# Kernel optimization log

Hardware: AMD Instinct MI355X
Metric: run time of the kernel (lower is better)

The kernel has to match this reference:

```python
import jax, jax.numpy as jnp
import numpy as np

CHUNK = 64
EPS = 1e-5


def segsum(a):
    # a: (..., T) -> (..., T, T) lower-triangular cumulative segment sums; -inf above diag
    T = a.shape[-1]
    cs = jnp.cumsum(a, axis=-1)
    ss = cs[..., :, None] - cs[..., None, :]
    mask = jnp.tril(jnp.ones((T, T), dtype=bool))
    return jnp.where(mask, ss, -jnp.inf)


def ssd(x, A, B, C, chunk):
    # x: (b, L, h, p), A: (b, L, h), B/C: (b, L, n)
    b, L, h, p = x.shape
    c = L // chunk
    x = x.reshape(b, c, chunk, h, p)
    A = A.reshape(b, c, chunk, h).transpose(0, 3, 1, 2)          # b h c l
    B = B.reshape(b, c, chunk, -1)                               # b c l n
    C = C.reshape(b, c, chunk, -1)                               # b c l n
    A_cum = jnp.cumsum(A, axis=-1)                               # b h c l
    Lmat = jnp.exp(segsum(A))                                    # b h c l l (causal decay)
    # intra-chunk (diagonal-block) output
    Y_diag = jnp.einsum('bcln,bcsn,bhcls,bcshp->bclhp', C, B, Lmat, x)
    # per-chunk states
    decay_states = jnp.exp(A_cum[..., -1:] - A_cum)              # b h c l
    states = jnp.einsum('bcln,bhcl,bclhp->bchpn', B, decay_states, x)
    states = jnp.concatenate([jnp.zeros_like(states[:, :1]), states], axis=1)  # b (c+1) h p n
    # inter-chunk recurrence via chunk-level segsum
    A_last = jnp.pad(A_cum[..., -1], ((0, 0), (0, 0), (1, 0)))   # b h (c+1)
    decay_chunk = jnp.exp(segsum(A_last))                        # b h (c+1) (c+1)
    new_states = jnp.einsum('bhzc,bchpn->bzhpn', decay_chunk, states)
    states, final = new_states[:, :-1], new_states[:, -1:]
    Y_off = jnp.einsum('bcln,bchpn,bhcl->bclhp', C, states, jnp.exp(A_cum))
    return (Y_diag + Y_off).reshape(b, L, h, p), final


def mamba2(x, W_in, conv_w, conv_b, dt_bias, A_log, D, norm_w, W_out):
    d_inner = norm_w.shape[0]
    nheads = dt_bias.shape[0]
    d_state = (conv_b.shape[0] - d_inner) // 2
    headdim = d_inner // nheads
    k_conv = conv_w.shape[0]
    b, L, _ = x.shape

    zxbcdt = x @ W_in                                            # (b, L, 2*d_inner+2*n+h)
    z = zxbcdt[..., :d_inner]
    xBC = zxbcdt[..., d_inner:2 * d_inner + 2 * d_state]
    dt = jax.nn.softplus(zxbcdt[..., 2 * d_inner + 2 * d_state:] + dt_bias)  # (b, L, h)
    A = -jnp.exp(A_log)                                          # (h,)

    # causal depthwise conv (zero init conv state == left-pad k_conv-1 zeros) + silu
    xp = jnp.pad(xBC, ((0, 0), (k_conv - 1, 0), (0, 0)))
    xBC = jax.lax.conv_general_dilated(
        xp, conv_w, (1,), 'VALID',
        dimension_numbers=('NWC', 'WIO', 'NWC'),
        feature_group_count=conv_b.shape[0])
    xBC = jax.nn.silu(xBC + conv_b)

    xs = xBC[..., :d_inner].reshape(b, L, nheads, headdim)       # (b, L, h, p)
    Bm = xBC[..., d_inner:d_inner + d_state]                     # (b, L, n)
    Cm = xBC[..., d_inner + d_state:]                            # (b, L, n)

    Y, _ = ssd(xs * dt[..., None], A * dt, Bm, Cm, CHUNK)
    Y = Y + xs * D                                               # D: (h, 1) broadcasts over p
    y = Y.reshape(b, L, d_inner)

    # gated RMSNorm
    y = y * jax.nn.silu(z)
    y = y * jax.lax.rsqrt(jnp.mean(y * y, axis=-1, keepdims=True) + EPS) * norm_w
    return y @ W_out


def setup_inputs():
    key = jax.random.key(0)
    ks = jax.random.split(key, 8)
    B, L, d_model = 2, 4096, 1024
    expand, d_state, k_conv, headdim = 2, 128, 4, 64
    d_inner = expand * d_model
    nheads = d_inner // headdim
    d_in_proj = 2 * d_inner + 2 * d_state + nheads
    conv_dim = d_inner + 2 * d_state
    return {
        'x': jax.random.normal(ks[0], (B, L, d_model), jnp.float32),
        'W_in': jax.random.normal(ks[1], (d_model, d_in_proj), jnp.float32) / np.sqrt(d_model).astype(np.float32),
        'conv_w': jax.random.normal(ks[2], (k_conv, 1, conv_dim), jnp.float32) / np.sqrt(k_conv).astype(np.float32),
        'conv_b': jnp.zeros((conv_dim,), jnp.float32),
        'dt_bias': jax.random.normal(ks[3], (nheads,), jnp.float32) * 0.5 - 2.0,
        'A_log': jnp.log(1.0 + 15.0 * jax.random.uniform(ks[4], (nheads,), jnp.float32)),
        'D': jax.random.normal(ks[5], (nheads, 1), jnp.float32),
        'norm_w': jnp.ones((d_inner,), jnp.float32),
        'W_out': jax.random.normal(ks[6], (d_inner, d_model), jnp.float32) / np.sqrt(d_inner).astype(np.float32),
    }


def reference(x, W_in, conv_w, conv_b, dt_bias, A_log, D, norm_w, W_out):
    return mamba2(x, W_in, conv_w, conv_b, dt_bias, A_log, D, norm_w, W_out)
```

## Files before the change

### kernel.cpp

```cpp
#include <hip/hip_runtime.h>
#include <hip/hip_fp16.h>

typedef _Float16 f16;
typedef _Float16 f16x4 __attribute__((ext_vector_type(4)));
typedef _Float16 f16x8 __attribute__((ext_vector_type(8)));
typedef float f32x4 __attribute__((ext_vector_type(4)));

#define DEV __device__ __forceinline__

constexpr int BB    = 2;
constexpr int LL    = 4096;
constexpr int DM    = 1024;
constexpr int DIN   = 2048;
constexpr int DST   = 128;
constexpr int NH    = 32;
constexpr int HD    = 64;
constexpr int NC    = 64;
constexpr int MROWS = BB * LL;
constexpr int NPROJ = 2*DIN + 2*DST + NH;
constexpr int NZ    = 2*DIN + 2*DST;
constexpr int CONVD = DIN + 2*DST;
constexpr int DT_OFF = 2*DIN + 2*DST;
constexpr int BOFF  = DIN;
constexpr int COFF  = DIN + DST;

DEV float silu_f(float v) { return v / (1.f + __expf(-v)); }

DEV void gload_lds16(const f16* gsrc, f16* lds_dst) {
  __builtin_amdgcn_global_load_lds(
      (const __attribute__((address_space(1))) void*)gsrc,
      (__attribute__((address_space(3))) void*)lds_dst, 16, 0, 0);
}

__global__ __launch_bounds__(256)
void tof16_kernel(const float* __restrict__ src, f16* __restrict__ dst, int n8) {
  int i = blockIdx.x * 256 + threadIdx.x;
  if (i >= n8) return;
  f32x4 a = *(const f32x4*)(src + (size_t)i*8);
  f32x4 b = *(const f32x4*)(src + (size_t)i*8 + 4);
  f16x8 o;
#pragma unroll
  for (int j = 0; j < 4; ++j) { o[j] = (f16)a[j]; o[4+j] = (f16)b[j]; }
  *(f16x8*)(dst + (size_t)i*8) = o;
}

__global__ __launch_bounds__(256)
void transpose_f32_to_f16(const float* __restrict__ src, f16* __restrict__ dst,
                          int K, int N, int srcLd) {
  __shared__ float tbuf[32][33];
  int n0 = blockIdx.x * 32, k0 = blockIdx.y * 32;
  int tx = threadIdx.x & 31, ty = threadIdx.x >> 5;
  for (int i = ty; i < 32; i += 8)
    tbuf[i][tx] = src[(size_t)(k0 + i)*srcLd + n0 + tx];
  __syncthreads();
  for (int i = ty; i < 32; i += 8)
    dst[(size_t)(n0 + i)*K + (k0 + tx)] = (f16)tbuf[tx][i];
}

template<int BM, int BN, int WM_, int WN_, bool C16>
__global__ __launch_bounds__(WM_*WN_*64, 2)
void gemm_t(const f16* __restrict__ A, const f16* __restrict__ Bt,
            void* __restrict__ Cp, int M, int N, int K, int ldc) {
  constexpr int THREADS = WM_*WN_*64;
  constexpr int WTM = BM/WM_, WTN = BN/WN_;
  constexpr int FM = WTM/16, FN = WTN/16;
  constexpr int LA = BM*4/THREADS, LB = BN*4/THREADS;
  constexpr int L = LA + LB;
  __shared__ f16 As[3][BM*32];
  __shared__ f16 Bs[3][BN*32];
  const int nbn = N / BN;
  const int bm = blockIdx.x / nbn, bn = blockIdx.x % nbn;
  const int tid = threadIdx.x;
  const int wave = tid >> 6, lane = tid & 63;
  const int lrow = lane & 15, kgrp = lane >> 4;
  const int wm = wave / WN_, wn = wave % WN_;
  const int nt = K >> 5;
  const int bcol8 = (kgrp ^ ((lrow ^ (lrow >> 2)) & 3)) * 8;

  const f16* aptr[LA];
  const f16* bptr[LB];
#pragma unroll
  for (int i = 0; i < LA; ++i) {
    int s = tid + i*THREADS, row = s >> 2;
    int g = (s & 3) ^ ((row ^ (row >> 2)) & 3);
    aptr[i] = A + (size_t)(bm*BM + row)*K + g*8;
  }
#pragma unroll
  for (int i = 0; i < LB; ++i) {
    int s = tid + i*THREADS, row = s >> 2;
    int g = (s & 3) ^ ((row ^ (row >> 2)) & 3);
    bptr[i] = Bt + (size_t)(bn*BN + row)*K + g*8;
  }

  f32x4 acc[FM][FN] = {};

  auto STAGE = [&](int buf, int t) {
#pragma unroll
    for (int i = 0; i < LA; ++i)
      gload_lds16(aptr[i] + (size_t)t*32, As[buf] + (wave*64 + i*THREADS)*8);
#pragma unroll
    for (int i = 0; i < LB; ++i)
      gload_lds16(bptr[i] + (size_t)t*32, Bs[buf] + (wave*64 + i*THREADS)*8);
  };
  auto WAITL = [&]() {
    if constexpr (L == 2)      asm volatile("s_waitcnt vmcnt(2)" ::: "memory");
    else if constexpr (L == 3) asm volatile("s_waitcnt vmcnt(3)" ::: "memory");
    else if constexpr (L == 4) asm volatile("s_waitcnt vmcnt(4)" ::: "memory");
    else if constexpr (L == 6) asm volatile("s_waitcnt vmcnt(6)" ::: "memory");
    else                       asm volatile("s_waitcnt vmcnt(0)" ::: "memory");
  };

  STAGE(0, 0);
  if (nt > 1) { STAGE(1, 1); WAITL(); }
  else        { asm volatile("s_waitcnt vmcnt(0)" ::: "memory"); }
  __builtin_amdgcn_s_barrier();
  __builtin_amdgcn_sched_barrier(0);

  for (int t = 0; t < nt; ++t) {
    const int cur = t % 3;
    if (t + 2 < nt) STAGE((t + 2) % 3, t + 2);
    const f16* Ab = As[cur];
    const f16* Bb = Bs[cur];
    f16x8 bf[FN];
#pragma unroll
    for (int n = 0; n < FN; ++n)
      bf[n] = *(const f16x8*)(Bb + (wn*WTN + n*16 + lrow)*32 + bcol8);
#pragma unroll
    for (int m = 0; m < FM; ++m) {
      f16x8 af = *(const f16x8*)(Ab + (wm*WTM + m*16 + lrow)*32 + bcol8);
#pragma unroll
      for (int n = 0; n < FN; ++n)
        acc[m][n] = __builtin_amdgcn_mfma_f32_16x16x32_f16(af, bf[n], acc[m][n], 0, 0, 0);
    }
    if (t + 1 < nt) {
      if (t + 2 < nt) WAITL();
      else            asm volatile("s_waitcnt vmcnt(0)" ::: "memory");
      __builtin_amdgcn_s_barrier();
      __builtin_amdgcn_sched_barrier(0);
    }
  }

  int crow0 = bm*BM + wm*WTM, ccol0 = bn*BN + wn*WTN;
#pragma unroll
  for (int m = 0; m < FM; ++m)
#pragma unroll
    for (int n = 0; n < FN; ++n) {
      int r0 = crow0 + m*16 + (lane >> 4)*4;
      int c0 = ccol0 + n*16 + (lane & 15);
#pragma unroll
      for (int r = 0; r < 4; ++r) {
        if constexpr (C16) {
          f16* C = (f16*)Cp;
          C[(size_t)(r0 + r)*ldc + c0] = (f16)acc[m][n][r];
        } else {
          float* C = (float*)Cp;
          C[(size_t)(r0 + r)*ldc + c0] = acc[m][n][r];
        }
      }
    }
}

__global__ __launch_bounds__(256)
void dt_kernel(const float* __restrict__ x, const float* __restrict__ Win,
               const float* __restrict__ dt_bias, const float* __restrict__ A_log,
               float* __restrict__ dt, float* __restrict__ Acum) {
  __shared__ float xs[64][132];
  __shared__ float ws[128][32];
  __shared__ float dts[64][32];
  int bc = blockIdx.x;
  int r0 = bc * 64;
  int t = threadIdx.x;
  int r = t >> 2, c0 = (t & 3) * 8;
  float acc[8] = {};
  for (int kt = 0; kt < 1024; kt += 128) {
    __syncthreads();
#pragma unroll
    for (int i = 0; i < 8; ++i) {
      int idx4 = t + i*256;
      int rr = idx4 >> 5, c4 = (idx4 & 31) * 4;
      *(f32x4*)&xs[rr][c4] = *(const f32x4*)(x + (size_t)(r0 + rr)*1024 + kt + c4);
    }
#pragma unroll
    for (int i = 0; i < 4; ++i) {
      int idx4 = t + i*256;
      int rr = idx4 >> 3, c4 = (idx4 & 7) * 4;
      *(f32x4*)&ws[rr][c4] = *(const f32x4*)(Win + (size_t)(kt + rr)*NPROJ + DT_OFF + c4);
    }
    __syncthreads();
#pragma unroll 8
    for (int k = 0; k < 128; ++k) {
      float xv = xs[r][k];
      f32x4 w0 = *(const f32x4*)&ws[k][c0];
      f32x4 w1 = *(const f32x4*)&ws[k][c0 + 4];
#pragma unroll
      for (int j = 0; j < 4; ++j) { acc[j] += xv * w0[j]; acc[4+j] += xv * w1[j]; }
    }
  }
#pragma unroll
  for (int j = 0; j < 8; ++j) {
    float v = acc[j] + dt_bias[c0 + j];
    float sp = (v > 20.f) ? v : log1pf(__expf(v));
    dt[(size_t)(r0 + r)*NH + c0 + j] = sp;
    dts[r][c0 + j] = sp;
  }
  __syncthreads();
  int wave = t >> 6, lane = t & 63;
  for (int hh = 0; hh < 8; ++hh) {
    int h = wave*8 + hh;
    float A = -__expf(A_log[h]);
    float v = A * dts[lane][h];
#pragma unroll
    for (int off = 1; off < 64; off <<= 1) {
      float u = __shfl_up(v, off);
      if (lane >= off) v += u;
    }
    Acum[((size_t)bc*NH + h)*64 + lane] = v;
  }
}

__global__ __launch_bounds__(256)
void conv_kernel(const f16* __restrict__ zxh, const float* __restrict__ cw,
                 const float* __restrict__ cb, f16* __restrict__ out) {
  int i = blockIdx.x * 256 + threadIdx.x;
  int row = i / (CONVD/8);
  int c8  = (i - row*(CONVD/8)) * 8;
  int lb = row & (LL - 1);
  f32x4 a0 = *(const f32x4*)(cb + c8);
  f32x4 a1 = *(const f32x4*)(cb + c8 + 4);
#pragma unroll
  for (int j = 0; j < 4; ++j) {
    int lsrc = lb - 3 + j;
    if (lsrc >= 0) {
      f16x8 v = *(const f16x8*)(zxh + (size_t)(row - 3 + j)*NZ + BOFF + c8);
      f32x4 w0 = *(const f32x4*)(cw + j*CONVD + c8);
      f32x4 w1 = *(const f32x4*)(cw + j*CONVD + c8 + 4);
#pragma unroll
      for (int jj = 0; jj < 4; ++jj) {
        a0[jj] += (float)v[jj]   * w0[jj];
        a1[jj] += (float)v[4+jj] * w1[jj];
      }
    }
  }
  f16x8 o;
#pragma unroll
  for (int jj = 0; jj < 4; ++jj) {
    o[jj]   = (f16)silu_f(a0[jj]);
    o[4+jj] = (f16)silu_f(a1[jj]);
  }
  *(f16x8*)(out + (size_t)row*CONVD + c8) = o;
}

__global__ __launch_bounds__(256)
void gbuf_kernel(const f16* __restrict__ xbc, f16* __restrict__ G) {
  __shared__ float Cs[64][128];
  __shared__ float Bsm[64][128];
  int bc = blockIdx.x;
  int row0 = bc * 64;
  int t = threadIdx.x;
#pragma unroll
  for (int i = 0; i < 4; ++i) {
    int idx = t + i*256;
    int r = idx >> 4, c8 = (idx & 15) * 8;
    f16x8 cv = *(const f16x8*)(xbc + (size_t)(row0 + r)*CONVD + COFF + c8);
    f16x8 bv = *(const f16x8*)(xbc + (size_t)(row0 + r)*CONVD + BOFF + c8);
    f32x4 c0v = {(float)cv[0], (float)cv[1], (float)cv[2], (float)cv[3]};
    f32x4 c1v = {(float)cv[4], (float)cv[5], (float)cv[6], (float)cv[7]};
    f32x4 b0v = {(float)bv[0], (float)bv[1], (float)bv[2], (float)bv[3]};
    f32x4 b1v = {(float)bv[4], (float)bv[5], (float)bv[6], (float)bv[7]};
    *(f32x4*)&Cs[r][c8]      = c0v;  *(f32x4*)&Cs[r][c8 + 4]  = c1v;
    *(f32x4*)&Bsm[r][c8]     = b0v;  *(f32x4*)&Bsm[r][c8 + 4] = b1v;
  }
  __syncthreads();
  int l0 = (t >> 4)*4, s0 = (t & 15)*4;
  float acc[4][4] = {};
  for (int n4 = 0; n4 < 128; n4 += 4) {
    f32x4 cv[4], bv[4];
#pragma unroll
    for (int i = 0; i < 4; ++i) cv[i] = *(const f32x4*)&Cs[l0 + i][n4];
#pragma unroll
    for (int j = 0; j < 4; ++j) bv[j] = *(const f32x4*)&Bsm[s0 + j][n4];
#pragma unroll
    for (int i = 0; i < 4; ++i)
#pragma unroll
      for (int j = 0; j < 4; ++j)
        acc[i][j] += cv[i][0]*bv[j][0] + cv[i][1]*bv[j][1] + cv[i][2]*bv[j][2] + cv[i][3]*bv[j][3];
  }
#pragma unroll
  for (int i = 0; i < 4; ++i) {
    f16x4 v = {(f16)acc[i][0], (f16)acc[i][1], (f16)acc[i][2], (f16)acc[i][3]};
    *(f16x4*)(G + ((size_t)bc*64 + l0 + i)*64 + s0) = v;
  }
}

__global__ __launch_bounds__(256)
void ssd_states_kernel(const f16* __restrict__ xbc, const float* __restrict__ dtb,
                       const float* __restrict__ Acum, f16* __restrict__ states) {
  __shared__ union {
    struct { f16 XdT[64][72]; f16 BT[128][72]; } s;
    float Sl[64][132];
  } u;
  __shared__ float ac[64], dts[64];
  int bc = blockIdx.x >> 5, h = blockIdx.x & 31;
  int row0 = bc*64, t = threadIdx.x;
  if (t < 64) {
    ac[t]  = Acum[((size_t)bc*NH + h)*64 + t];
    dts[t] = dtb[(size_t)(row0 + t)*NH + h];
  }
  __syncthreads();
  float ac63 = ac[63];
#pragma unroll
  for (int i = 0; i < 2; ++i) {
    int idx = t + i*256; int l = idx >> 3, p8 = (idx & 7)*8;
    f16x8 v = *(const f16x8*)(xbc + (size_t)(row0 + l)*CONVD + h*HD + p8);
    float d = dts[l];
#pragma unroll
    for (int j = 0; j < 8; ++j) u.s.XdT[p8 + j][l] = (f16)((float)v[j]*d);
  }
#pragma unroll
  for (int i = 0; i < 4; ++i) {
    int idx = t + i*256; int l = idx >> 4, n8 = (idx & 15)*8;
    f16x8 v = *(const f16x8*)(xbc + (size_t)(row0 + l)*CONVD + BOFF + n8);
    float dl = __expf(ac63 - ac[l]);
#pragma unroll
    for (int j = 0; j < 8; ++j) u.s.BT[n8 + j][l] = (f16)((float)v[j]*dl);
  }
  __syncthreads();
  int wave = t >> 6, lane = t & 63;
  int lrow = lane & 15, kgrp = lane >> 4;
  f32x4 sacc[8] = {};
#pragma unroll
  for (int kk = 0; kk < 64; kk += 32) {
    f16x8 afs = *(const f16x8*)&u.s.XdT[wave*16 + lrow][kk + kgrp*8];
#pragma unroll
    for (int n = 0; n < 8; ++n) {
      f16x8 bf = *(const f16x8*)&u.s.BT[n*16 + lrow][kk + kgrp*8];
      sacc[n] = __builtin_amdgcn_mfma_f32_16x16x32_f16(afs, bf, sacc[n], 0, 0, 0);
    }
  }
  __syncthreads();
#pragma unroll
  for (int n = 0; n < 8; ++n)
#pragma unroll
    for (int r = 0; r < 4; ++r)
      u.Sl[wave*16 + kgrp*4 + r][n*16 + lrow] = sacc[n][r];
  __syncthreads();
  size_t sb = ((size_t)bc*NH + h)*8192;
#pragma unroll
  for (int i = 0; i < 4; ++i) {
    int idx = t + i*256; int p = idx >> 4, n8 = (idx & 15)*8;
    f16x8 o;
#pragma unroll
    for (int j = 0; j < 8; ++j) o[j] = (f16)u.Sl[p][n8 + j];
    *(f16x8*)(states + sb + (size_t)p*128 + n8) = o;
  }
}

__global__ __launch_bounds__(256)
void scan_kernel(f16* __restrict__ states, const float* __restrict__ Acum) {
  int bid = blockIdx.x;
  int bh = bid >> 3, pgrp = bid & 7;
  int b = bh >> 5, h = bh & 31;
  int t = threadIdx.x;
  int p = pgrp*8 + (t >> 5), n4 = (t & 31) * 4;
  size_t off = (size_t)p*128 + n4;
  f32x4 carry = {0.f, 0.f, 0.f, 0.f};
  for (int c = 0; c < NC; ++c) {
    size_t base = ((size_t)(b*NC + c)*NH + h)*8192;
    f16x4 cv = *(f16x4*)(states + base + off);
    f16x4 st;
#pragma unroll
    for (int j = 0; j < 4; ++j) st[j] = (f16)carry[j];
    *(f16x4*)(states + base + off) = st;
    float tc = __expf(Acum[((size_t)(b*NC + c)*NH + h)*64 + 63]);
#pragma unroll
    for (int j = 0; j < 4; ++j) carry[j] = carry[j]*tc + (float)cv[j];
  }
}

__global__ __launch_bounds__(256)
void yoff_kernel(const f16* __restrict__ xbc, const f16* __restrict__ zxh,
                 const f16* __restrict__ Gg, const f16* __restrict__ states,
                 const float* __restrict__ dtb, const float* __restrict__ Acum,
                 const float* __restrict__ Dp, f16* __restrict__ Ybuf) {
  __shared__ union {
    struct { f16 Gt[64][72]; f16 XdT[64][72]; } a;
    struct { f16 Ch[64][136]; f16 Sin[64][136]; } b;
    float Yl2[64][68];
  } u;
  __shared__ float Yl[64][68];
  __shared__ float ac[64], dts[64], eac[64];
  int bc = blockIdx.x >> 5, h = blockIdx.x & 31;
  int row0 = bc*64, t = threadIdx.x;
  if (t < 64) {
    float a0 = Acum[((size_t)bc*NH + h)*64 + t];
    ac[t]  = a0;
    eac[t] = __expf(a0);
    dts[t] = dtb[(size_t)(row0 + t)*NH + h];
  }
  __syncthreads();
#pragma unroll
  for (int i = 0; i < 2; ++i) {
    int idx = t + i*256; int l = idx >> 3, p8 = (idx & 7)*8;
    f16x8 v = *(const f16x8*)(xbc + (size_t)(row0 + l)*CONVD + h*HD + p8);
    float d = dts[l];
#pragma unroll
    for (int j = 0; j < 8; ++j) u.a.XdT[p8 + j][l] = (f16)((float)v[j]*d);
  }
#pragma unroll
  for (int i = 0; i < 2; ++i) {
    int idx = t + i*256; int l = idx >> 3, s8 = (idx & 7)*8;
    f16x8 g = *(const f16x8*)(Gg + (size_t)bc*4096 + l*64 + s8);
    float al = ac[l];
    f16x8 o;
#pragma unroll
    for (int j = 0; j < 8; ++j) {
      int s = s8 + j;
      o[j] = (l >= s) ? (f16)((float)g[j] * __expf(al - ac[s])) : (f16)0.f;
    }
    *(f16x8*)&u.a.Gt[l][s8] = o;
  }
  __syncthreads();
  int wave = t >> 6, lane = t & 63;
  int lrow = lane & 15, kgrp = lane >> 4;
  f32x4 yacc[4] = {};
#pragma unroll
  for (int kk = 0; kk < 64; kk += 32) {
    f16x8 afy = *(const f16x8*)&u.a.Gt[wave*16 + lrow][kk + kgrp*8];
#pragma unroll
    for (int n = 0; n < 4; ++n) {
      f16x8 bf = *(const f16x8*)&u.a.XdT[n*16 + lrow][kk + kgrp*8];
      yacc[n] = __builtin_amdgcn_mfma_f32_16x16x32_f16(afy, bf, yacc[n], 0, 0, 0);
    }
  }
  __syncthreads();
#pragma unroll
  for (int n = 0; n < 4; ++n)
#pragma unroll
    for (int r = 0; r < 4; ++r)
      Yl[wave*16 + kgrp*4 + r][n*16 + lrow] = yacc[n][r];
  size_t sb = ((size_t)bc*NH + h)*8192;
#pragma unroll
  for (int i = 0; i < 4; ++i) {
    int idx = t + i*256; int r = idx >> 4, c8 = (idx & 15)*8;
    *(f16x8*)&u.b.Ch[r][c8]  = *(const f16x8*)(xbc + (size_t)(row0 + r)*CONVD + COFF + c8);
    *(f16x8*)&u.b.Sin[r][c8] = *(const f16x8*)(states + sb + (size_t)r*128 + c8);
  }
  __syncthreads();
  f32x4 acc[4] = {};
#pragma unroll
  for (int kk = 0; kk < 128; kk += 32) {
    f16x8 af = *(const f16x8*)&u.b.Ch[wave*16 + lrow][kk + kgrp*8];
#pragma unroll
    for (int n = 0; n < 4; ++n) {
      f16x8 bf = *(const f16x8*)&u.b.Sin[n*16 + lrow][kk + kgrp*8];
      acc[n] = __builtin_amdgcn_mfma_f32_16x16x32_f16(af, bf, acc[n], 0, 0, 0);
    }
  }
  __syncthreads();
#pragma unroll
  for (int n = 0; n < 4; ++n)
#pragma unroll
    for (int r = 0; r < 4; ++r)
      u.Yl2[wave*16 + kgrp*4 + r][n*16 + lrow] = acc[n][r];
  __syncthreads();
  float Dh = Dp[h];
#pragma unroll
  for (int i = 0; i < 2; ++i) {
    int idx = t + i*256; int l = idx >> 3, p8 = (idx & 7)*8;
    int row = row0 + l;
    f16x8 zh = *(const f16x8*)(zxh + (size_t)row*NZ + h*HD + p8);
    f16x8 xs = *(const f16x8*)(xbc + (size_t)row*CONVD + h*HD + p8);
    float e = eac[l];
    f16x8 o;
#pragma unroll
    for (int j = 0; j < 8; ++j) {
      float yv = Yl[l][p8 + j] + e*u.Yl2[l][p8 + j] + (float)xs[j]*Dh;
      o[j] = (f16)(yv * silu_f((float)zh[j]));
    }
    *(f16x8*)(Ybuf + (size_t)row*DIN + h*HD + p8) = o;
  }
}

__global__ __launch_bounds__(256)
void rms_kernel(const f16* __restrict__ yg, const float* __restrict__ nw,
                f16* __restrict__ yh) {
  __shared__ float red[4];
  int row = blockIdx.x, t = threadIdx.x;
  f16x8 v = *(const f16x8*)(yg + (size_t)row*DIN + t*8);
  float f[8];
  float ss = 0.f;
#pragma unroll
  for (int j = 0; j < 8; ++j) { f[j] = (float)v[j]; ss += f[j]*f[j]; }
#pragma unroll
  for (int off = 32; off > 0; off >>= 1) ss += __shfl_down(ss, off);
  if ((t & 63) == 0) red[t >> 6] = ss;
  __syncthreads();
  float tot = red[0] + red[1] + red[2] + red[3];
  float sc = rsqrtf(tot * (1.f/2048.f) + 1e-5f);
  f32x4 w0 = *(const f32x4*)(nw + t*8);
  f32x4 w1 = *(const f32x4*)(nw + t*8 + 4);
  f16x8 o;
#pragma unroll
  for (int j = 0; j < 4; ++j) {
    o[j]   = (f16)(f[j]   * sc * w0[j]);
    o[4+j] = (f16)(f[4+j] * sc * w1[j]);
  }
  *(f16x8*)(yh + (size_t)row*DIN + t*8) = o;
}

extern "C" void kernel_launch(void* const* d_in, const int* in_sizes, int n_in,
                              void* d_out, int out_size, void* d_ws, size_t ws_size,
                              hipStream_t stream) {
  const float* x       = (const float*)d_in[0];
  const float* W_in    = (const float*)d_in[1];
  const float* conv_w  = (const float*)d_in[2];
  const float* conv_b  = (const float*)d_in[3];
  const float* dt_bias = (const float*)d_in[4];
  const float* A_log   = (const float*)d_in[5];
  const float* Dp      = (const float*)d_in[6];
  const float* norm_w  = (const float*)d_in[7];
  const float* W_out   = (const float*)d_in[8];

  constexpr size_t WS_NEED = 213909504;
  if (ws_size < WS_NEED) return;

  char* w = (char*)d_ws;
  f16*   states = (f16*)(w + 0);
  f16*   winT   = (f16*)(w + 0);
  f16*   yh     = (f16*)(w + 0);
  f16*   xh     = (f16*)(w + 33554432);
  f16*   woutT  = (f16*)(w + 33554432);
  f16*   zxh    = (f16*)(w + 67108864);
  f16*   xbcc   = (f16*)(w + 138412032);
  f16*   Ybuf   = (f16*)(w + 176160768);
  float* dtb    = (float*)(w + 209715200);
  float* Acum   = (float*)(w + 210763776);
  f16*   Gg     = (f16*)(w + 211812352);

  tof16_kernel<<<4096, 256, 0, stream>>>(x, xh, MROWS*DM/8);
  transpose_f32_to_f16<<<dim3(NZ/32, DM/32), 256, 0, stream>>>(W_in, winT, DM, NZ, NPROJ);
  gemm_t<256,128,4,2,true><<<(MROWS/256)*(NZ/128), 512, 0, stream>>>(xh, winT, zxh, MROWS, NZ, DM, NZ);
  dt_kernel<<<MROWS/64, 256, 0, stream>>>(x, W_in, dt_bias, A_log, dtb, Acum);
  conv_kernel<<<MROWS*(CONVD/8)/256, 256, 0, stream>>>(zxh, conv_w, conv_b, xbcc);
  gbuf_kernel<<<BB*NC, 256, 0, stream>>>(xbcc, Gg);
  ssd_states_kernel<<<BB*NC*NH, 256, 0, stream>>>(xbcc, dtb, Acum, states);
  scan_kernel<<<BB*NH*8, 256, 0, stream>>>(states, Acum);
  yoff_kernel<<<BB*NC*NH, 256, 0, stream>>>(xbcc, zxh, Gg, states, dtb, Acum, Dp, Ybuf);
  transpose_f32_to_f16<<<dim3(DM/32, DIN/32), 256, 0, stream>>>(W_out, woutT, DIN, DM, DM);
  rms_kernel<<<MROWS, 256, 0, stream>>>(Ybuf, norm_w, yh);
  gemm_t<128,128,2,2,false><<<(MROWS/128)*(DM/128), 256, 0, stream>>>(yh, woutT, d_out, MROWS, DM, DIN, DM);
}
```

Baseline: 434.9 us.

## Fold RMSNorm weight into W_out and row scale into GEMM epilogue; remap GEMM blocks

The norm weight is folded into the transposed W_out, and the RMS normalization becomes a per-row scale applied in the output GEMM's epilogue. The rms kernel now only computes the scale, so the normalized f16 copy of Y is no longer written and re-read. Both GEMMs also remap block indices with an interleave across groups of 8 workgroups, probably to spread neighbouring tiles across XCDs or improve cache locality. The GEMM now reads the unnormalized f16 Y, which is a small numeric difference, and the epilogue does an extra scale load per row.

```diff
diff --git a/kernel.cpp b/kernel.cpp
--- a/kernel.cpp
+++ b/kernel.cpp
@@ -46,21 +46,23 @@
 
 __global__ __launch_bounds__(256)
 void transpose_f32_to_f16(const float* __restrict__ src, f16* __restrict__ dst,
-                          int K, int N, int srcLd) {
+                          int K, int N, int srcLd, const float* __restrict__ colScale) {
   __shared__ float tbuf[32][33];
   int n0 = blockIdx.x * 32, k0 = blockIdx.y * 32;
   int tx = threadIdx.x & 31, ty = threadIdx.x >> 5;
   for (int i = ty; i < 32; i += 8)
     tbuf[i][tx] = src[(size_t)(k0 + i)*srcLd + n0 + tx];
   __syncthreads();
+  float cs = colScale ? colScale[k0 + tx] : 1.f;
   for (int i = ty; i < 32; i += 8)
-    dst[(size_t)(n0 + i)*K + (k0 + tx)] = (f16)tbuf[tx][i];
+    dst[(size_t)(n0 + i)*K + (k0 + tx)] = (f16)(tbuf[tx][i] * cs);
 }
 
 template<int BM, int BN, int WM_, int WN_, bool C16>
 __global__ __launch_bounds__(WM_*WN_*64, 2)
 void gemm_t(const f16* __restrict__ A, const f16* __restrict__ Bt,
-            void* __restrict__ Cp, int M, int N, int K, int ldc) {
+            void* __restrict__ Cp, int M, int N, int K, int ldc,
+            const float* __restrict__ rowScale) {
   constexpr int THREADS = WM_*WN_*64;
   constexpr int WTM = BM/WM_, WTN = BN/WN_;
   constexpr int FM = WTM/16, FN = WTN/16;
@@ -69,7 +71,9 @@
   __shared__ f16 As[3][BM*32];
   __shared__ f16 Bs[3][BN*32];
   const int nbn = N / BN;
-  const int bm = blockIdx.x / nbn, bn = blockIdx.x % nbn;
+  const int nwg = (int)gridDim.x;
+  const int lb  = ((int)blockIdx.x & 7) * (nwg >> 3) + ((int)blockIdx.x >> 3);
+  const int bm = lb / nbn, bn = lb % nbn;
   const int tid = threadIdx.x;
   const int wave = tid >> 6, lane = tid & 63;
   const int lrow = lane & 15, kgrp = lane >> 4;
@@ -149,12 +153,14 @@
       int c0 = ccol0 + n*16 + (lane & 15);
 #pragma unroll
       for (int r = 0; r < 4; ++r) {
+        float v = acc[m][n][r];
+        if (rowScale) v *= rowScale[r0 + r];
         if constexpr (C16) {
           f16* C = (f16*)Cp;
-          C[(size_t)(r0 + r)*ldc + c0] = (f16)acc[m][n][r];
+          C[(size_t)(r0 + r)*ldc + c0] = (f16)v;
         } else {
           float* C = (float*)Cp;
-          C[(size_t)(r0 + r)*ldc + c0] = acc[m][n][r];
+          C[(size_t)(r0 + r)*ldc + c0] = v;
         }
       }
     }
@@ -482,30 +488,21 @@
 }
 
 __global__ __launch_bounds__(256)
-void rms_kernel(const f16* __restrict__ yg, const float* __restrict__ nw,
-                f16* __restrict__ yh) {
+void rms_scale_kernel(const f16* __restrict__ yg, float* __restrict__ scale) {
   __shared__ float red[4];
   int row = blockIdx.x, t = threadIdx.x;
   f16x8 v = *(const f16x8*)(yg + (size_t)row*DIN + t*8);
-  float f[8];
   float ss = 0.f;
 #pragma unroll
-  for (int j = 0; j < 8; ++j) { f[j] = (float)v[j]; ss += f[j]*f[j]; }
+  for (int j = 0; j < 8; ++j) { float f = (float)v[j]; ss += f*f; }
 #pragma unroll
   for (int off = 32; off > 0; off >>= 1) ss += __shfl_down(ss, off);
   if ((t & 63) == 0) red[t >> 6] = ss;
   __syncthreads();
-  float tot = red[0] + red[1] + red[2] + red[3];
-  float sc = rsqrtf(tot * (1.f/2048.f) + 1e-5f);
-  f32x4 w0 = *(const f32x4*)(nw + t*8);
-  f32x4 w1 = *(const f32x4*)(nw + t*8 + 4);
-  f16x8 o;
-#pragma unroll
-  for (int j = 0; j < 4; ++j) {
-    o[j]   = (f16)(f[j]   * sc * w0[j]);
-    o[4+j] = (f16)(f[4+j] * sc * w1[j]);
-  }
-  *(f16x8*)(yh + (size_t)row*DIN + t*8) = o;
+  if (t == 0) {
+    float tot = red[0] + red[1] + red[2] + red[3];
+    scale[row] = rsqrtf(tot * (1.f/2048.f) + 1e-5f);
+  }
 }
 
 extern "C" void kernel_launch(void* const* d_in, const int* in_sizes, int n_in,
@@ -527,7 +524,6 @@
   char* w = (char*)d_ws;
   f16*   states = (f16*)(w + 0);
   f16*   winT   = (f16*)(w + 0);
-  f16*   yh     = (f16*)(w + 0);
   f16*   xh     = (f16*)(w + 33554432);
   f16*   woutT  = (f16*)(w + 33554432);
   f16*   zxh    = (f16*)(w + 67108864);
@@ -536,17 +532,18 @@
   float* dtb    = (float*)(w + 209715200);
   float* Acum   = (float*)(w + 210763776);
   f16*   Gg     = (f16*)(w + 211812352);
+  float* rscale = (float*)(w + 212860928);
 
   tof16_kernel<<<4096, 256, 0, stream>>>(x, xh, MROWS*DM/8);
-  transpose_f32_to_f16<<<dim3(NZ/32, DM/32), 256, 0, stream>>>(W_in, winT, DM, NZ, NPROJ);
-  gemm_t<256,128,4,2,true><<<(MROWS/256)*(NZ/128), 512, 0, stream>>>(xh, winT, zxh, MROWS, NZ, DM, NZ);
+  transpose_f32_to_f16<<<dim3(NZ/32, DM/32), 256, 0, stream>>>(W_in, winT, DM, NZ, NPROJ, nullptr);
+  gemm_t<256,128,4,2,true><<<(MROWS/256)*(NZ/128), 512, 0, stream>>>(xh, winT, zxh, MROWS, NZ, DM, NZ, nullptr);
   dt_kernel<<<MROWS/64, 256, 0, stream>>>(x, W_in, dt_bias, A_log, dtb, Acum);
   conv_kernel<<<MROWS*(CONVD/8)/256, 256, 0, stream>>>(zxh, conv_w, conv_b, xbcc);
   gbuf_kernel<<<BB*NC, 256, 0, stream>>>(xbcc, Gg);
   ssd_states_kernel<<<BB*NC*NH, 256, 0, stream>>>(xbcc, dtb, Acum, states);
   scan_kernel<<<BB*NH*8, 256, 0, stream>>>(states, Acum);
   yoff_kernel<<<BB*NC*NH, 256, 0, stream>>>(xbcc, zxh, Gg, states, dtb, Acum, Dp, Ybuf);
-  transpose_f32_to_f16<<<dim3(DM/32, DIN/32), 256, 0, stream>>>(W_out, woutT, DIN, DM, DM);
-  rms_kernel<<<MROWS, 256, 0, stream>>>(Ybuf, norm_w, yh);
-  gemm_t<128,128,2,2,false><<<(MROWS/128)*(DM/128), 256, 0, stream>>>(yh, woutT, d_out, MROWS, DM, DIN, DM);
-}
+  transpose_f32_to_f16<<<dim3(DM/32, DIN/32), 256, 0, stream>>>(W_out, woutT, DIN, DM, DM, norm_w);
+  rms_scale_kernel<<<MROWS, 256, 0, stream>>>(Ybuf, rscale);
+  gemm_t<128,128,2,2,false><<<(MROWS/128)*(DM/128), 256, 0, stream>>>(Ybuf, woutT, d_out, MROWS, DM, DIN, DM, rscale);
+}
```

After: 430.4 us. About the same (-1.0%).
